# Kernel optimization log

Hardware: AMD Instinct MI355X
Metric: run time of the kernel (lower is better)

## Reference

```python
import jax, jax.numpy as jnp
import numpy as np
from jax import lax

# ---- model dims (from init_kwargs) ----
H_SIZE = 2048      # hidden_size
NK = 16            # linear_num_key_heads
NV = 32            # linear_num_value_heads
DK = 128           # linear_key_head_dim
DV = 128           # linear_value_head_dim
KCONV = 4          # linear_conv_kernel_dim
KEY_DIM = NK * DK          # 2048
VAL_DIM = NV * DV          # 4096
CONV_DIM = 2 * KEY_DIM + VAL_DIM  # 8192
B, S = 2, 2048
EPS = 1e-6


def _l2norm(x, eps=EPS):
    return x * lax.rsqrt(jnp.sum(x * x, axis=-1, keepdims=True) + eps)


def setup_inputs() -> dict:
    key = jax.random.key(0)
    ks = jax.random.split(key, 7)
    x = jax.random.normal(ks[0], (B, S, H_SIZE), jnp.float32)
    W_qkvz = jax.random.normal(ks[1], (2 * KEY_DIM + 2 * VAL_DIM, H_SIZE), jnp.float32) * 0.02
    W_ba = jax.random.normal(ks[2], (2 * NV, H_SIZE), jnp.float32) * 0.02
    conv_w = jax.random.normal(ks[3], (CONV_DIM, 1, KCONV), jnp.float32) * 0.2  # depthwise OIH
    dt_bias = jnp.ones((NV,), jnp.float32)
    A_log = jnp.log(jax.random.uniform(ks[4], (NV,), jnp.float32, 1e-3, 16.0))
    norm_w = jnp.zeros((VAL_DIM,), jnp.float32)
    W_out = jax.random.normal(ks[5], (H_SIZE, VAL_DIM), jnp.float32) * 0.02
    return {"x": x, "W_qkvz": W_qkvz, "W_ba": W_ba, "conv_w": conv_w,
            "dt_bias": dt_bias, "A_log": A_log, "norm_w": norm_w, "W_out": W_out}


def reference(x, W_qkvz, W_ba, conv_w, dt_bias, A_log, norm_w, W_out):
    bs, s, _ = x.shape
    qkvz = jnp.einsum('bsh,ph->bsp', x, W_qkvz)
    ba = jnp.einsum('bsh,ph->bsp', x, W_ba)
    q, k, v, z = jnp.split(qkvz, [KEY_DIM, 2 * KEY_DIM, 2 * KEY_DIM + VAL_DIM], axis=-1)
    b, a = jnp.split(ba, [NV], axis=-1)

    # causal depthwise conv1d over channels (left pad K-1), then SiLU
    mixed = jnp.concatenate([q, k, v], axis=-1).transpose(0, 2, 1)  # [B, CONV_DIM, S]
    mixed = lax.conv_general_dilated(
        mixed, conv_w, window_strides=(1,), padding=[(KCONV - 1, 0)],
        dimension_numbers=('NCH', 'OIH', 'NCH'), feature_group_count=CONV_DIM)
    mixed = jax.nn.silu(mixed).transpose(0, 2, 1)  # [B, S, CONV_DIM]
    q, k, v = jnp.split(mixed, [KEY_DIM, 2 * KEY_DIM], axis=-1)

    q = q.reshape(bs, s, NK, DK)
    k = k.reshape(bs, s, NK, DK)
    v = v.reshape(bs, s, NV, DV)
    beta = jax.nn.sigmoid(b)                                   # [B,S,NV]
    g = -jnp.exp(A_log) * jax.nn.softplus(a + dt_bias)         # [B,S,NV]

    rep = NV // NK
    if rep > 1:
        q = jnp.repeat(q, rep, axis=2)
        k = jnp.repeat(k, rep, axis=2)
    q = _l2norm(q).astype(jnp.float32)
    k = _l2norm(k).astype(jnp.float32)
    v = v.astype(jnp.float32)

    # time-major for scan: [S, B, H, d]
    qs = q.transpose(1, 0, 2, 3)
    ks_ = k.transpose(1, 0, 2, 3)
    vs = v.transpose(1, 0, 2, 3)
    ge = jnp.exp(g).transpose(1, 0, 2)      # [S,B,H]
    bs_ = beta.astype(jnp.float32).transpose(1, 0, 2)  # [S,B,H]

    state0 = jnp.zeros((bs, NV, DK, DV), jnp.float32)

    def step(state, ts):
        q_t, k_t, v_t, g_t, b_t = ts
        state = state * g_t[..., None, None]
        kv_mem = jnp.einsum('bhk,bhkv->bhv', k_t, state)
        delta = b_t[..., None] * (v_t - kv_mem)
        state = state + jnp.einsum('bhk,bhv->bhkv', k_t, delta)
        o_t = jnp.einsum('bhk,bhkv->bhv', q_t, state)
        return state, o_t

    _, core = lax.scan(step, state0, (qs, ks_, vs, ge, bs_))  # core: [S,B,H,DV]
    core = core.transpose(1, 0, 2, 3).reshape(bs, s, VAL_DIM)

    # RMSNorm with (1 + weight) scale
    core = core * lax.rsqrt(jnp.mean(core * core, axis=-1, keepdims=True) + EPS)
    core = core * (1.0 + norm_w)
    core = core * jax.nn.silu(z)
    return jnp.einsum('bsv,hv->bsh', core, W_out)
```

## Files before the change

### kernel.cpp

```cpp
#include <hip/hip_runtime.h>
#include <hip/hip_bf16.h>
#include <math.h>

#define TOK    4096
#define HS     2048
#define CONVD  8192
#define KEYD   2048
#define VALD   4096
#define NKH    16
#define NVH    32
#define DKH    128
#define DVH    128
#define SEQ    2048
#define NBATCH 2
#define EPSF   1e-6f
#define CHUNK  64
#define NCHUNK 32

typedef __attribute__((ext_vector_type(8))) short short8;
typedef __attribute__((ext_vector_type(4))) float floatx4;

static __device__ __forceinline__ unsigned short f2bf(float x) {
  union { float f; unsigned u; } c; c.f = x;
  unsigned r = (c.u + 0x7FFF + ((c.u >> 16) & 1)) >> 16;
  return (unsigned short)r;
}
static __device__ __forceinline__ float bf2f(unsigned short u) {
  union { unsigned u; float f; } c; c.u = ((unsigned)u) << 16;
  return c.f;
}

__global__ __launch_bounds__(256) void gemm_nt(
    const float* __restrict__ A, const float* __restrict__ B,
    float* __restrict__ C, int M, int N, int K) {
  __shared__ float As[16][68];
  __shared__ float Bs[16][68];
  const int tx = threadIdx.x & 15;
  const int ty = threadIdx.x >> 4;
  const int row0 = blockIdx.y * 64;
  const int col0 = blockIdx.x * 64;
  const int lr = threadIdx.x >> 2;
  const int lc = (threadIdx.x & 3) * 4;
  float acc[4][4] = {};
  for (int k0 = 0; k0 < K; k0 += 16) {
    float4 av = *(const float4*)&A[(size_t)(row0 + lr) * K + (k0 + lc)];
    float4 bv = *(const float4*)&B[(size_t)(col0 + lr) * K + (k0 + lc)];
    As[lc + 0][lr] = av.x; As[lc + 1][lr] = av.y;
    As[lc + 2][lr] = av.z; As[lc + 3][lr] = av.w;
    Bs[lc + 0][lr] = bv.x; Bs[lc + 1][lr] = bv.y;
    Bs[lc + 2][lr] = bv.z; Bs[lc + 3][lr] = bv.w;
    __syncthreads();
    #pragma unroll
    for (int kk = 0; kk < 16; kk++) {
      float a[4], b[4];
      #pragma unroll
      for (int i = 0; i < 4; i++) a[i] = As[kk][ty * 4 + i];
      #pragma unroll
      for (int i = 0; i < 4; i++) b[i] = Bs[kk][tx * 4 + i];
      #pragma unroll
      for (int i = 0; i < 4; i++)
        #pragma unroll
        for (int j = 0; j < 4; j++)
          acc[i][j] += a[i] * b[j];
    }
    __syncthreads();
  }
  #pragma unroll
  for (int i = 0; i < 4; i++) {
    float4 v = make_float4(acc[i][0], acc[i][1], acc[i][2], acc[i][3]);
    *(float4*)&C[(size_t)(row0 + ty * 4 + i) * N + (col0 + tx * 4)] = v;
  }
}

__global__ __launch_bounds__(256) void cast_bf16(
    const float4* __restrict__ src, ushort4* __restrict__ dst, int n4) {
  int i = blockIdx.x * 256 + threadIdx.x;
  if (i < n4) {
    float4 v = src[i];
    ushort4 o;
    o.x = f2bf(v.x); o.y = f2bf(v.y); o.z = f2bf(v.z); o.w = f2bf(v.w);
    dst[i] = o;
  }
}

__global__ __launch_bounds__(256) void gemm_bf16_nt(
    const ushort* __restrict__ A, const ushort* __restrict__ B,
    float* __restrict__ C, int M, int N, int K) {
  __shared__ ushort Asm[128 * 32];
  __shared__ ushort Bsm[128 * 32];
  const int tid = threadIdx.x;
  const int w = tid >> 6, l = tid & 63;
  const int row0 = blockIdx.y * 128, col0 = blockIdx.x * 128;
  const int wm = w >> 1, wn = w & 1;

  floatx4 acc[4][4];
  #pragma unroll
  for (int i = 0; i < 4; i++)
    #pragma unroll
    for (int j = 0; j < 4; j++)
      acc[i][j] = (floatx4){0.f, 0.f, 0.f, 0.f};

  const int srow = w * 16 + (l >> 2);
  const int scol = (l & 3) * 8;
  const ushort* Ag = A + (size_t)(row0 + srow) * K + scol;
  const ushort* Bg = B + (size_t)(col0 + srow) * K + scol;

  for (int k0 = 0; k0 < K; k0 += 32) {
    #pragma unroll
    for (int c = 0; c < 2; c++) {
      __builtin_amdgcn_global_load_lds(
          (const __attribute__((address_space(1))) void*)(Ag + (size_t)(c * 64) * K + k0),
          (__attribute__((address_space(3))) void*)&Asm[(c * 64 + w * 16) * 32],
          16, 0, 0);
      __builtin_amdgcn_global_load_lds(
          (const __attribute__((address_space(1))) void*)(Bg + (size_t)(c * 64) * K + k0),
          (__attribute__((address_space(3))) void*)&Bsm[(c * 64 + w * 16) * 32],
          16, 0, 0);
    }
    __syncthreads();
    short8 af[4], bfv[4];
    #pragma unroll
    for (int i = 0; i < 4; i++) {
      af[i]  = *(const short8*)&Asm[(wm * 64 + i * 16 + (l & 15)) * 32 + (l >> 4) * 8];
      bfv[i] = *(const short8*)&Bsm[(wn * 64 + i * 16 + (l & 15)) * 32 + (l >> 4) * 8];
    }
    #pragma unroll
    for (int i = 0; i < 4; i++)
      #pragma unroll
      for (int j = 0; j < 4; j++)
        acc[i][j] = __builtin_amdgcn_mfma_f32_16x16x32_bf16(af[i], bfv[j], acc[i][j], 0, 0, 0);
    __syncthreads();
  }

  const int cl = l & 15, rq = l >> 4;
  #pragma unroll
  for (int i = 0; i < 4; i++) {
    int r0 = row0 + wm * 64 + i * 16 + rq * 4;
    #pragma unroll
    for (int j = 0; j < 4; j++) {
      int cc = col0 + wn * 64 + j * 16 + cl;
      #pragma unroll
      for (int r = 0; r < 4; r++)
        C[(size_t)(r0 + r) * N + cc] = acc[i][j][r];
    }
  }
}

__global__ __launch_bounds__(256) void conv_silu(
    const float* __restrict__ qkv, const float* __restrict__ cw,
    float* __restrict__ mix) {
  size_t idx = (size_t)blockIdx.x * 256 + threadIdx.x;
  int c = (int)(idx % CONVD);
  size_t t = idx / CONVD;
  int s = (int)(t % SEQ);
  float w0 = cw[c * 4 + 0], w1 = cw[c * 4 + 1], w2 = cw[c * 4 + 2], w3 = cw[c * 4 + 3];
  const float* col = qkv + t * CONVD + c;
  float acc = w3 * col[0];
  if (s >= 1) acc += w2 * col[-(ptrdiff_t)CONVD];
  if (s >= 2) acc += w1 * col[-2 * (ptrdiff_t)CONVD];
  if (s >= 3) acc += w0 * col[-3 * (ptrdiff_t)CONVD];
  float sig = 1.f / (1.f + expf(-acc));
  mix[t * CONVD + c] = acc * sig;
}

__global__ __launch_bounds__(256) void gates_kernel(
    const float* __restrict__ ba, const float* __restrict__ A_log,
    const float* __restrict__ dt_bias, float2* __restrict__ g2) {
  int idx = blockIdx.x * 256 + threadIdx.x;
  int h = idx & 31;
  size_t t = (size_t)(idx >> 5);
  float bv = ba[t * 64 + h];
  float av = ba[t * 64 + 32 + h];
  float beta = 1.f / (1.f + expf(-bv));
  float xx = av + dt_bias[h];
  float sp = (xx > 20.f) ? xx : log1pf(expf(xx));
  float lg = -expf(A_log[h]) * sp;
  g2[t * 32 + h] = make_float2(lg, beta);
}

__global__ __launch_bounds__(256) void l2norm_qk(float* __restrict__ mix) {
  int wid = (blockIdx.x * 256 + threadIdx.x) >> 6;
  int lane = threadIdx.x & 63;
  size_t t = (size_t)(wid >> 5);
  int hh = wid & 31;
  float* p = mix + t * CONVD + (size_t)hh * DKH;
  float v0 = p[lane], v1 = p[lane + 64];
  float ss = v0 * v0 + v1 * v1;
  #pragma unroll
  for (int off = 32; off >= 1; off >>= 1) ss += __shfl_xor(ss, off, 64);
  float sc = rsqrtf(ss + EPSF);
  p[lane] = v0 * sc;
  p[lane + 64] = v1 * sc;
}

__global__ __launch_bounds__(64) void chunk_prep(
    const float* __restrict__ mix, const float2* __restrict__ g2,
    float* __restrict__ Lgbuf, ushort* __restrict__ Tbuf,
    ushort* __restrict__ Mbuf) {
  const int blk = blockIdx.x;
  const int ch = blk & 31;
  const int h  = (blk >> 5) & 31;
  const int b  = blk >> 10;
  const int kh = h >> 1;
  const int l  = threadIdx.x;
  const int fr = l & 15;
  const int fc8 = (l >> 4) * 8;
  const int cr = (l >> 4) * 4;

  __shared__ float sLg[64], sB[64];
  __shared__ float sA[64 * 65];
  __shared__ float sT[64 * 65];

  float2 gv = g2[((size_t)(b * SEQ + ch * 64 + l)) * 32 + h];
  float lg = gv.x;
  #pragma unroll
  for (int off = 1; off < 64; off <<= 1) {
    float n = __shfl_up(lg, off, 64);
    if (l >= off) lg += n;
  }
  sLg[l] = lg; sB[l] = gv.y;
  Lgbuf[(size_t)blk * 64 + l] = lg;
  __syncthreads();

  const float* kb = mix + ((size_t)(b * SEQ + ch * 64)) * CONVD + KEYD + (size_t)kh * DKH;
  const float* qb = mix + ((size_t)(b * SEQ + ch * 64)) * CONVD + (size_t)kh * DKH;

  floatx4 zero4 = {0.f, 0.f, 0.f, 0.f};
  floatx4 kk[4][4], qk[4][4];
  #pragma unroll
  for (int i = 0; i < 4; i++)
    #pragma unroll
    for (int j = 0; j < 4; j++) { kk[i][j] = zero4; qk[i][j] = zero4; }

  for (int ks = 0; ks < 4; ks++) {
    short8 kf[4], qf[4];
    #pragma unroll
    for (int m = 0; m < 4; m++) {
      const float* kp = kb + (size_t)(m * 16 + fr) * CONVD + fc8 + ks * 32;
      const float* qp = qb + (size_t)(m * 16 + fr) * CONVD + fc8 + ks * 32;
      float4 a0 = *(const float4*)kp, a1 = *(const float4*)(kp + 4);
      float4 c0 = *(const float4*)qp, c1 = *(const float4*)(qp + 4);
      short8 kv, qv;
      kv[0]=(short)f2bf(a0.x); kv[1]=(short)f2bf(a0.y); kv[2]=(short)f2bf(a0.z); kv[3]=(short)f2bf(a0.w);
      kv[4]=(short)f2bf(a1.x); kv[5]=(short)f2bf(a1.y); kv[6]=(short)f2bf(a1.z); kv[7]=(short)f2bf(a1.w);
      qv[0]=(short)f2bf(c0.x); qv[1]=(short)f2bf(c0.y); qv[2]=(short)f2bf(c0.z); qv[3]=(short)f2bf(c0.w);
      qv[4]=(short)f2bf(c1.x); qv[5]=(short)f2bf(c1.y); qv[6]=(short)f2bf(c1.z); qv[7]=(short)f2bf(c1.w);
      kf[m] = kv; qf[m] = qv;
    }
    #pragma unroll
    for (int mt = 0; mt < 4; mt++)
      #pragma unroll
      for (int nt = 0; nt < 4; nt++) {
        kk[mt][nt] = __builtin_amdgcn_mfma_f32_16x16x32_bf16(kf[mt], kf[nt], kk[mt][nt], 0, 0, 0);
        qk[mt][nt] = __builtin_amdgcn_mfma_f32_16x16x32_bf16(qf[mt], kf[nt], qk[mt][nt], 0, 0, 0);
      }
  }

  const size_t tmbase = (size_t)blk * 4096;
  #pragma unroll
  for (int mt = 0; mt < 4; mt++)
    #pragma unroll
    for (int r = 0; r < 4; r++) {
      int i = mt * 16 + cr + r;
      float Li = sLg[i], Bi = sB[i];
      #pragma unroll
      for (int nt = 0; nt < 4; nt++) {
        int j = nt * 16 + fr;
        float dec = expf(Li - sLg[j]);
        sA[i * 65 + j] = (j < i) ? Bi * dec * kk[mt][nt][r] : 0.f;
        float mv = (j <= i) ? dec * qk[mt][nt][r] : 0.f;
        Mbuf[tmbase + (size_t)i * 64 + j] = f2bf(mv);
      }
    }
  __syncthreads();

  sT[0 * 65 + l] = (l == 0) ? 1.f : 0.f;
  for (int i = 1; i < 64; i++) {
    float acc = (l == i) ? 1.f : 0.f;
    for (int j = 0; j < i; j++)
      acc -= sA[i * 65 + j] * sT[j * 65 + l];
    sT[i * 65 + l] = acc;
  }
  for (int i = 0; i < 64; i++)
    Tbuf[tmbase + (size_t)i * 64 + l] = f2bf(sT[i * 65 + l]);
}

__global__ __launch_bounds__(256) void chunk_scan(
    const float* __restrict__ mix, const float2* __restrict__ g2,
    const float* __restrict__ Lgbuf, const ushort* __restrict__ Tbuf,
    const ushort* __restrict__ Mbuf, float* __restrict__ core) {
  const int blk = blockIdx.x;
  const int vq = blk & 3;
  const int bh = blk >> 2;
  const int h = bh & 31;
  const int b = bh >> 5;
  const int kh = h >> 1;
  const int tid = threadIdx.x;
  const int w = tid >> 6;
  const int l = tid & 63;
  const int fr = l & 15;
  const int fc8 = (l >> 4) * 8;
  const int cr = (l >> 4) * 4;

  __shared__ ushort STh[32][136], STl[32][136];
  __shared__ ushort DTh[32][72],  DTl[32][72];
  __shared__ float sKB[64], sQv[64], sKh[64], sBe[64];
  __shared__ float sLgC;

  for (int i = tid; i < 32 * 136; i += 256) { (&STh[0][0])[i] = 0; (&STl[0][0])[i] = 0; }

  floatx4 zero4 = {0.f, 0.f, 0.f, 0.f};
  floatx4 sacc[2][2] = {{zero4, zero4}, {zero4, zero4}};

  const size_t mixb = (size_t)b * SEQ * CONVD;
  const float* kbase = mix + mixb + KEYD + (size_t)kh * DKH;
  const float* qbase = mix + mixb + (size_t)kh * DKH;
  const float* vbase = mix + mixb + 2 * KEYD + (size_t)h * DVH + vq * 32;
  float* cbase = core + (size_t)b * SEQ * VALD + (size_t)h * DVH + vq * 32;

  for (int ch = 0; ch < NCHUNK; ch++) {
    const int tok0 = ch * 64;
    const size_t tmbase = ((size_t)bh * 32 + ch) * 4096;
    if (tid < 64) {
      float Lgv = Lgbuf[((size_t)bh * 32 + ch) * 64 + tid];
      float LgC = Lgbuf[((size_t)bh * 32 + ch) * 64 + 63];
      float2 gv = g2[((size_t)(b * SEQ + tok0 + tid)) * 32 + h];
      float e = expf(Lgv);
      sKB[tid] = gv.y * e;
      sQv[tid] = e;
      sKh[tid] = expf(LgC - Lgv);
      sBe[tid] = gv.y;
      if (tid == 0) sLgC = LgC;
    }
    __syncthreads();

    const int ia = w * 16 + fr;
    floatx4 p[2] = {zero4, zero4};
    {
      const float* arow = kbase + (size_t)(tok0 + ia) * CONVD;
      float ascl = sKB[ia];
      #pragma unroll
      for (int ks = 0; ks < 4; ks++) {
        float4 x0 = *(const float4*)(arow + fc8 + ks * 32);
        float4 x1 = *(const float4*)(arow + fc8 + ks * 32 + 4);
        short8 af;
        af[0]=(short)f2bf(x0.x*ascl); af[1]=(short)f2bf(x0.y*ascl);
        af[2]=(short)f2bf(x0.z*ascl); af[3]=(short)f2bf(x0.w*ascl);
        af[4]=(short)f2bf(x1.x*ascl); af[5]=(short)f2bf(x1.y*ascl);
        af[6]=(short)f2bf(x1.z*ascl); af[7]=(short)f2bf(x1.w*ascl);
        #pragma unroll
        for (int nt = 0; nt < 2; nt++) {
          short8 bh_ = *(const short8*)&STh[nt * 16 + fr][fc8 + ks * 32];
          short8 bl_ = *(const short8*)&STl[nt * 16 + fr][fc8 + ks * 32];
          p[nt] = __builtin_amdgcn_mfma_f32_16x16x32_bf16(af, bh_, p[nt], 0, 0, 0);
          p[nt] = __builtin_amdgcn_mfma_f32_16x16x32_bf16(af, bl_, p[nt], 0, 0, 0);
        }
      }
    }
    #pragma unroll
    for (int nt = 0; nt < 2; nt++)
      #pragma unroll
      for (int r = 0; r < 4; r++) {
        int i = w * 16 + cr + r;
        int v = nt * 16 + fr;
        float vv = vbase[(size_t)(tok0 + i) * CONVD + v];
        float Rv = sBe[i] * vv - p[nt][r];
        unsigned short hv = f2bf(Rv);
        DTh[v][i] = hv;
        DTl[v][i] = f2bf(Rv - bf2f(hv));
      }
    __syncthreads();

    floatx4 d[2] = {zero4, zero4};
    #pragma unroll
    for (int ks = 0; ks < 2; ks++) {
      short8 af = *(const short8*)&Tbuf[tmbase + (size_t)ia * 64 + fc8 + ks * 32];
      #pragma unroll
      for (int nt = 0; nt < 2; nt++) {
        short8 bh_ = *(const short8*)&DTh[nt * 16 + fr][fc8 + ks * 32];
        short8 bl_ = *(const short8*)&DTl[nt * 16 + fr][fc8 + ks * 32];
        d[nt] = __builtin_amdgcn_mfma_f32_16x16x32_bf16(af, bh_, d[nt], 0, 0, 0);
        d[nt] = __builtin_amdgcn_mfma_f32_16x16x32_bf16(af, bl_, d[nt], 0, 0, 0);
      }
    }
    __syncthreads();
    #pragma unroll
    for (int nt = 0; nt < 2; nt++)
      #pragma unroll
      for (int r = 0; r < 4; r++) {
        int i = w * 16 + cr + r;
        int v = nt * 16 + fr;
        float dv = d[nt][r];
        unsigned short hv = f2bf(dv);
        DTh[v][i] = hv;
        DTl[v][i] = f2bf(dv - bf2f(hv));
      }
    __syncthreads();

    floatx4 o[2] = {zero4, zero4};
    {
      const float* arow = qbase + (size_t)(tok0 + ia) * CONVD;
      float ascl = sQv[ia];
      #pragma unroll
      for (int ks = 0; ks < 4; ks++) {
        float4 x0 = *(const float4*)(arow + fc8 + ks * 32);
        float4 x1 = *(const float4*)(arow + fc8 + ks * 32 + 4);
        short8 af;
        af[0]=(short)f2bf(x0.x*ascl); af[1]=(short)f2bf(x0.y*ascl);
        af[2]=(short)f2bf(x0.z*ascl); af[3]=(short)f2bf(x0.w*ascl);
        af[4]=(short)f2bf(x1.x*ascl); af[5]=(short)f2bf(x1.y*ascl);
        af[6]=(short)f2bf(x1.z*ascl); af[7]=(short)f2bf(x1.w*ascl);
        #pragma unroll
        for (int nt = 0; nt < 2; nt++) {
          short8 bh_ = *(const short8*)&STh[nt * 16 + fr][fc8 + ks * 32];
          short8 bl_ = *(const short8*)&STl[nt * 16 + fr][fc8 + ks * 32];
          o[nt] = __builtin_amdgcn_mfma_f32_16x16x32_bf16(af, bh_, o[nt], 0, 0, 0);
          o[nt] = __builtin_amdgcn_mfma_f32_16x16x32_bf16(af, bl_, o[nt], 0, 0, 0);
        }
      }
      #pragma unroll
      for (int ks = 0; ks < 2; ks++) {
        short8 af = *(const short8*)&Mbuf[tmbase + (size_t)ia * 64 + fc8 + ks * 32];
        #pragma unroll
        for (int nt = 0; nt < 2; nt++) {
          short8 bh_ = *(const short8*)&DTh[nt * 16 + fr][fc8 + ks * 32];
          short8 bl_ = *(const short8*)&DTl[nt * 16 + fr][fc8 + ks * 32];
          o[nt] = __builtin_amdgcn_mfma_f32_16x16x32_bf16(af, bh_, o[nt], 0, 0, 0);
          o[nt] = __builtin_amdgcn_mfma_f32_16x16x32_bf16(af, bl_, o[nt], 0, 0, 0);
        }
      }
    }
    #pragma unroll
    for (int nt = 0; nt < 2; nt++)
      #pragma unroll
      for (int r = 0; r < 4; r++) {
        int i = w * 16 + cr + r;
        int v = nt * 16 + fr;
        cbase[(size_t)(tok0 + i) * VALD + v] = o[nt][r];
      }

    float eL = expf(sLgC);
    #pragma unroll
    for (int mt = 0; mt < 2; mt++)
      #pragma unroll
      for (int nt = 0; nt < 2; nt++)
        sacc[mt][nt] = sacc[mt][nt] * eL;
    #pragma unroll
    for (int ks = 0; ks < 2; ks++) {
      float kh8[8];
      #pragma unroll
      for (int jj = 0; jj < 8; jj++) kh8[jj] = sKh[fc8 + ks * 32 + jj];
      short8 afm[2];
      #pragma unroll
      for (int mt = 0; mt < 2; mt++) {
        int krow = w * 32 + mt * 16 + fr;
        short8 a;
        #pragma unroll
        for (int jj = 0; jj < 8; jj++) {
          float kvv = kbase[(size_t)(tok0 + fc8 + ks * 32 + jj) * CONVD + krow];
          a[jj] = (short)f2bf(kvv * kh8[jj]);
        }
        afm[mt] = a;
      }
      #pragma unroll
      for (int mt = 0; mt < 2; mt++)
        #pragma unroll
        for (int nt = 0; nt < 2; nt++) {
          short8 bh_ = *(const short8*)&DTh[nt * 16 + fr][fc8 + ks * 32];
          short8 bl_ = *(const short8*)&DTl[nt * 16 + fr][fc8 + ks * 32];
          sacc[mt][nt] = __builtin_amdgcn_mfma_f32_16x16x32_bf16(afm[mt], bh_, sacc[mt][nt], 0, 0, 0);
          sacc[mt][nt] = __builtin_amdgcn_mfma_f32_16x16x32_bf16(afm[mt], bl_, sacc[mt][nt], 0, 0, 0);
        }
    }
    __syncthreads();
    #pragma unroll
    for (int mt = 0; mt < 2; mt++)
      #pragma unroll
      for (int nt = 0; nt < 2; nt++)
        #pragma unroll
        for (int r = 0; r < 4; r++) {
          int k = w * 32 + mt * 16 + cr + r;
          int v = nt * 16 + fr;
          float sv = sacc[mt][nt][r];
          unsigned short hv = f2bf(sv);
          STh[v][k] = hv;
          STl[v][k] = f2bf(sv - bf2f(hv));
        }
  }
}

__global__ __launch_bounds__(256) void rmsnorm_silu(
    const float* __restrict__ core, const float* __restrict__ zbuf,
    const float* __restrict__ norm_w, ushort* __restrict__ out_bf) {
  int t = blockIdx.x;
  int tid = threadIdx.x;
  const float* row = core + (size_t)t * VALD;
  const float* zrow = zbuf + (size_t)t * VALD;
  ushort* orow = out_bf + (size_t)t * VALD;
  float vals[16];
  float ss = 0.f;
  #pragma unroll
  for (int i = 0; i < 16; i++) { float x = row[tid + i * 256]; vals[i] = x; ss += x * x; }
  #pragma unroll
  for (int off = 32; off >= 1; off >>= 1) ss += __shfl_xor(ss, off, 64);
  __shared__ float red[4];
  if ((tid & 63) == 0) red[tid >> 6] = ss;
  __syncthreads();
  float tot = red[0] + red[1] + red[2] + red[3];
  float scale = rsqrtf(tot * (1.f / VALD) + EPSF);
  #pragma unroll
  for (int i = 0; i < 16; i++) {
    int c = tid + i * 256;
    float z = zrow[c];
    float sz = z / (1.f + expf(-z));
    orow[c] = f2bf(vals[i] * scale * (1.f + norm_w[c]) * sz);
  }
}

extern "C" void kernel_launch(void* const* d_in, const int* in_sizes, int n_in,
                              void* d_out, int out_size, void* d_ws, size_t ws_size,
                              hipStream_t stream) {
  const float* x       = (const float*)d_in[0];
  const float* W_qkvz  = (const float*)d_in[1];
  const float* W_ba    = (const float*)d_in[2];
  const float* conv_w  = (const float*)d_in[3];
  const float* dt_bias = (const float*)d_in[4];
  const float* A_log   = (const float*)d_in[5];
  const float* norm_w  = (const float*)d_in[6];
  const float* W_out   = (const float*)d_in[7];
  float* out = (float*)d_out;

  float* ws = (float*)d_ws;
  float* A  = ws;
  float* Bp = A + (size_t)33554432;
  float* Cp = Bp + (size_t)33554432;
  float* ba = Cp + (size_t)16777216;
  float* g2 = ba + (size_t)262144;

  ushort* x_bf    = (ushort*)Cp;
  ushort* Wqkv_bf = (ushort*)Bp;
  float*  zb      = A;
  ushort* core_bf = (ushort*)(A + (size_t)16777216);
  ushort* Wz_bf   = (ushort*)(A + (size_t)25165824);
  ushort* Wo_bf   = (ushort*)Bp;
  float*  mix     = Bp;
  float*  core    = Cp;
  ushort* Tbuf    = (ushort*)(A + (size_t)16777216);
  ushort* Mbuf    = (ushort*)(A + (size_t)20971520);
  float*  Lgbuf   = A + (size_t)29360128;

  cast_bf16<<<(TOK * HS / 4 + 255) / 256, 256, 0, stream>>>((const float4*)x, (ushort4*)x_bf, TOK * HS / 4);
  cast_bf16<<<(CONVD * HS / 4 + 255) / 256, 256, 0, stream>>>((const float4*)W_qkvz, (ushort4*)Wqkv_bf, CONVD * HS / 4);
  gemm_bf16_nt<<<dim3(CONVD / 128, TOK / 128), 256, 0, stream>>>(x_bf, Wqkv_bf, A, TOK, CONVD, HS);
  gemm_nt<<<dim3(1, TOK / 64), 256, 0, stream>>>(x, W_ba, ba, TOK, 64, HS);
  conv_silu<<<(int)(((size_t)TOK * CONVD) / 256), 256, 0, stream>>>(A, conv_w, mix);
  cast_bf16<<<(VALD * HS / 4 + 255) / 256, 256, 0, stream>>>(
      (const float4*)(W_qkvz + (size_t)(2 * KEYD + VALD) * HS), (ushort4*)Wz_bf, VALD * HS / 4);
  gemm_bf16_nt<<<dim3(VALD / 128, TOK / 128), 256, 0, stream>>>(x_bf, Wz_bf, zb, TOK, VALD, HS);
  gates_kernel<<<TOK * NVH / 256, 256, 0, stream>>>(ba, A_log, dt_bias, (float2*)g2);
  l2norm_qk<<<TOK * 32 / 4, 256, 0, stream>>>(mix);
  chunk_prep<<<NBATCH * NVH * NCHUNK, 64, 0, stream>>>(mix, (const float2*)g2, Lgbuf, Tbuf, Mbuf);
  chunk_scan<<<NBATCH * NVH * 4, 256, 0, stream>>>(mix, (const float2*)g2, Lgbuf, Tbuf, Mbuf, core);
  rmsnorm_silu<<<TOK, 256, 0, stream>>>(core, zb, norm_w, core_bf);
  cast_bf16<<<(HS * VALD / 4 + 255) / 256, 256, 0, stream>>>((const float4*)W_out, (ushort4*)Wo_bf, HS * VALD / 4);
  gemm_bf16_nt<<<dim3(HS / 128, TOK / 128), 256, 0, stream>>>(core_bf, Wo_bf, out, TOK, HS, VALD);
}
```

Before: 1.188 ms.

## Store normalized q/k as bf16 and software-pipeline chunk_scan with register prefetch

l2norm now writes the normalized q and k to a compact bf16 buffer instead of normalizing in place in fp32. chunk_prep and chunk_scan read that buffer directly, which removes repeated fp32 loads and conversions. chunk_scan is restructured to prefetch the next chunk's K rows and gate values into registers and to load Q/T/M/V early. K is staged in LDS so the transposed state-update reads come from shared memory rather than strided global loads. It also uses lighter barriers, packed LDS stores, and folds the key scaling into the residual, at the cost of extra registers (launch bounds set to one block per SM) and bf16 rounding of q/k before scaling.

Measured after the change: 1.106 ms. 6.9% less time.

```diff
diff --git a/kernel.cpp b/kernel.cpp
--- a/kernel.cpp
+++ b/kernel.cpp
@@ -29,6 +29,13 @@
   union { unsigned u; float f; } c; c.u = ((unsigned)u) << 16;
   return c.f;
 }
+
+#define BAR() do { \
+  __builtin_amdgcn_sched_barrier(0); \
+  asm volatile("s_waitcnt lgkmcnt(0)" ::: "memory"); \
+  __builtin_amdgcn_s_barrier(); \
+  __builtin_amdgcn_sched_barrier(0); \
+} while (0)
 
 __global__ __launch_bounds__(256) void gemm_nt(
     const float* __restrict__ A, const float* __restrict__ B,
@@ -178,23 +185,25 @@
   g2[t * 32 + h] = make_float2(lg, beta);
 }
 
-__global__ __launch_bounds__(256) void l2norm_qk(float* __restrict__ mix) {
+__global__ __launch_bounds__(256) void l2norm_qk(
+    const float* __restrict__ mix, ushort* __restrict__ kq) {
   int wid = (blockIdx.x * 256 + threadIdx.x) >> 6;
   int lane = threadIdx.x & 63;
   size_t t = (size_t)(wid >> 5);
   int hh = wid & 31;
-  float* p = mix + t * CONVD + (size_t)hh * DKH;
+  const float* p = mix + t * CONVD + (size_t)hh * DKH;
   float v0 = p[lane], v1 = p[lane + 64];
   float ss = v0 * v0 + v1 * v1;
   #pragma unroll
   for (int off = 32; off >= 1; off >>= 1) ss += __shfl_xor(ss, off, 64);
   float sc = rsqrtf(ss + EPSF);
-  p[lane] = v0 * sc;
-  p[lane + 64] = v1 * sc;
+  ushort* q = kq + t * 4096 + (size_t)hh * DKH;
+  q[lane] = f2bf(v0 * sc);
+  q[lane + 64] = f2bf(v1 * sc);
 }
 
 __global__ __launch_bounds__(64) void chunk_prep(
-    const float* __restrict__ mix, const float2* __restrict__ g2,
+    const ushort* __restrict__ kq, const float2* __restrict__ g2,
     float* __restrict__ Lgbuf, ushort* __restrict__ Tbuf,
     ushort* __restrict__ Mbuf) {
   const int blk = blockIdx.x;
@@ -222,8 +231,8 @@
   Lgbuf[(size_t)blk * 64 + l] = lg;
   __syncthreads();
 
-  const float* kb = mix + ((size_t)(b * SEQ + ch * 64)) * CONVD + KEYD + (size_t)kh * DKH;
-  const float* qb = mix + ((size_t)(b * SEQ + ch * 64)) * CONVD + (size_t)kh * DKH;
+  const ushort* qb = kq + ((size_t)(b * SEQ + ch * 64)) * 4096 + (size_t)kh * DKH;
+  const ushort* kb = qb + 2048;
 
   floatx4 zero4 = {0.f, 0.f, 0.f, 0.f};
   floatx4 kk[4][4], qk[4][4];
@@ -236,16 +245,8 @@
     short8 kf[4], qf[4];
     #pragma unroll
     for (int m = 0; m < 4; m++) {
-      const float* kp = kb + (size_t)(m * 16 + fr) * CONVD + fc8 + ks * 32;
-      const float* qp = qb + (size_t)(m * 16 + fr) * CONVD + fc8 + ks * 32;
-      float4 a0 = *(const float4*)kp, a1 = *(const float4*)(kp + 4);
-      float4 c0 = *(const float4*)qp, c1 = *(const float4*)(qp + 4);
-      short8 kv, qv;
-      kv[0]=(short)f2bf(a0.x); kv[1]=(short)f2bf(a0.y); kv[2]=(short)f2bf(a0.z); kv[3]=(short)f2bf(a0.w);
-      kv[4]=(short)f2bf(a1.x); kv[5]=(short)f2bf(a1.y); kv[6]=(short)f2bf(a1.z); kv[7]=(short)f2bf(a1.w);
-      qv[0]=(short)f2bf(c0.x); qv[1]=(short)f2bf(c0.y); qv[2]=(short)f2bf(c0.z); qv[3]=(short)f2bf(c0.w);
-      qv[4]=(short)f2bf(c1.x); qv[5]=(short)f2bf(c1.y); qv[6]=(short)f2bf(c1.z); qv[7]=(short)f2bf(c1.w);
-      kf[m] = kv; qf[m] = qv;
+      kf[m] = *(const short8*)(kb + (size_t)(m * 16 + fr) * 4096 + fc8 + ks * 32);
+      qf[m] = *(const short8*)(qb + (size_t)(m * 16 + fr) * 4096 + fc8 + ks * 32);
     }
     #pragma unroll
     for (int mt = 0; mt < 4; mt++)
@@ -285,10 +286,13 @@
     Tbuf[tmbase + (size_t)i * 64 + l] = f2bf(sT[i * 65 + l]);
 }
 
-__global__ __launch_bounds__(256) void chunk_scan(
-    const float* __restrict__ mix, const float2* __restrict__ g2,
-    const float* __restrict__ Lgbuf, const ushort* __restrict__ Tbuf,
-    const ushort* __restrict__ Mbuf, float* __restrict__ core) {
+struct KReg { short8 K[4]; float gLg, gB, gLgC; };
+
+__global__ __launch_bounds__(256, 1) void chunk_scan(
+    const float* __restrict__ mix, const ushort* __restrict__ kq,
+    const float2* __restrict__ g2, const float* __restrict__ Lgbuf,
+    const ushort* __restrict__ Tbuf, const ushort* __restrict__ Mbuf,
+    float* __restrict__ core) {
   const int blk = blockIdx.x;
   const int vq = blk & 3;
   const int bh = blk >> 2;
@@ -301,11 +305,13 @@
   const int fr = l & 15;
   const int fc8 = (l >> 4) * 8;
   const int cr = (l >> 4) * 4;
-
-  __shared__ ushort STh[32][136], STl[32][136];
-  __shared__ ushort DTh[32][72],  DTl[32][72];
-  __shared__ float sKB[64], sQv[64], sKh[64], sBe[64];
-  __shared__ float sLgC;
+  const int w16 = w * 16, w32 = w * 32;
+  const int ia = w16 + fr;
+
+  __shared__ __align__(16) ushort Kt[64][136];
+  __shared__ __align__(16) ushort STh[32][136], STl[32][136];
+  __shared__ __align__(16) ushort DTh[32][72],  DTl[32][72];
+  __shared__ float sKB[64], sQv[64], sKh[64], sBe[64], sLgC[1];
 
   for (int i = tid; i < 32 * 136; i += 256) { (&STh[0][0])[i] = 0; (&STl[0][0])[i] = 0; }
 
@@ -313,152 +319,160 @@
   floatx4 sacc[2][2] = {{zero4, zero4}, {zero4, zero4}};
 
   const size_t mixb = (size_t)b * SEQ * CONVD;
-  const float* kbase = mix + mixb + KEYD + (size_t)kh * DKH;
-  const float* qbase = mix + mixb + (size_t)kh * DKH;
-  const float* vbase = mix + mixb + 2 * KEYD + (size_t)h * DVH + vq * 32;
+  const float* vb = mix + mixb + 2 * KEYD + (size_t)h * DVH + vq * 32;
+  const ushort* kq_q = kq + (size_t)b * SEQ * 4096 + (size_t)kh * DKH;
+  const ushort* kq_k = kq_q + 2048;
+  const ushort* Tb = Tbuf + (size_t)bh * 32 * 4096;
+  const ushort* Mb = Mbuf + (size_t)bh * 32 * 4096;
+  const float* Lgb = Lgbuf + (size_t)bh * 2048;
+  const float2* gp = g2 + (size_t)b * SEQ * 32 + h;
   float* cbase = core + (size_t)b * SEQ * VALD + (size_t)h * DVH + vq * 32;
 
-  for (int ch = 0; ch < NCHUNK; ch++) {
+  auto kpre = [&](KReg& R, int ch) {
+    size_t ro = (size_t)(ch * 64 + ia) * 4096;
+    #pragma unroll
+    for (int ks = 0; ks < 4; ks++)
+      R.K[ks] = *(const short8*)(kq_k + ro + fc8 + ks * 32);
+    if (tid < 64) {
+      R.gLg = Lgb[ch * 64 + tid];
+      R.gLgC = Lgb[ch * 64 + 63];
+      R.gB = gp[(size_t)(ch * 64 + tid) * 32].y;
+    }
+  };
+
+  auto body = [&](KReg& cur, KReg& nxt, int ch) {
     const int tok0 = ch * 64;
-    const size_t tmbase = ((size_t)bh * 32 + ch) * 4096;
     if (tid < 64) {
-      float Lgv = Lgbuf[((size_t)bh * 32 + ch) * 64 + tid];
-      float LgC = Lgbuf[((size_t)bh * 32 + ch) * 64 + 63];
-      float2 gv = g2[((size_t)(b * SEQ + tok0 + tid)) * 32 + h];
-      float e = expf(Lgv);
-      sKB[tid] = gv.y * e;
+      float e = expf(cur.gLg);
+      sKB[tid] = cur.gB * e;
       sQv[tid] = e;
-      sKh[tid] = expf(LgC - Lgv);
-      sBe[tid] = gv.y;
-      if (tid == 0) sLgC = LgC;
-    }
-    __syncthreads();
-
-    const int ia = w * 16 + fr;
+      sKh[tid] = expf(cur.gLgC - cur.gLg);
+      sBe[tid] = cur.gB;
+      if (tid == 0) sLgC[0] = cur.gLgC;
+    }
+    #pragma unroll
+    for (int ks = 0; ks < 4; ks++)
+      *(short8*)&Kt[ia][fc8 + ks * 32] = cur.K[ks];
+    short8 Qr[4], Tr[2], Mr[2];
+    float Vr[8];
+    {
+      size_t ro = (size_t)(tok0 + ia) * 4096;
+      #pragma unroll
+      for (int ks = 0; ks < 4; ks++)
+        Qr[ks] = *(const short8*)(kq_q + ro + fc8 + ks * 32);
+      size_t tmb = (size_t)ch * 4096 + (size_t)ia * 64;
+      #pragma unroll
+      for (int ks = 0; ks < 2; ks++) {
+        Tr[ks] = *(const short8*)(Tb + tmb + fc8 + ks * 32);
+        Mr[ks] = *(const short8*)(Mb + tmb + fc8 + ks * 32);
+      }
+      #pragma unroll
+      for (int nt = 0; nt < 2; nt++)
+        #pragma unroll
+        for (int r = 0; r < 4; r++)
+          Vr[nt * 4 + r] = vb[(size_t)(tok0 + w16 + cr + r) * CONVD + nt * 16 + fr];
+    }
+    BAR();
+    kpre(nxt, (ch + 1 < NCHUNK) ? ch + 1 : NCHUNK - 1);
+
     floatx4 p[2] = {zero4, zero4};
-    {
-      const float* arow = kbase + (size_t)(tok0 + ia) * CONVD;
-      float ascl = sKB[ia];
-      #pragma unroll
-      for (int ks = 0; ks < 4; ks++) {
-        float4 x0 = *(const float4*)(arow + fc8 + ks * 32);
-        float4 x1 = *(const float4*)(arow + fc8 + ks * 32 + 4);
-        short8 af;
-        af[0]=(short)f2bf(x0.x*ascl); af[1]=(short)f2bf(x0.y*ascl);
-        af[2]=(short)f2bf(x0.z*ascl); af[3]=(short)f2bf(x0.w*ascl);
-        af[4]=(short)f2bf(x1.x*ascl); af[5]=(short)f2bf(x1.y*ascl);
-        af[6]=(short)f2bf(x1.z*ascl); af[7]=(short)f2bf(x1.w*ascl);
-        #pragma unroll
-        for (int nt = 0; nt < 2; nt++) {
-          short8 bh_ = *(const short8*)&STh[nt * 16 + fr][fc8 + ks * 32];
-          short8 bl_ = *(const short8*)&STl[nt * 16 + fr][fc8 + ks * 32];
-          p[nt] = __builtin_amdgcn_mfma_f32_16x16x32_bf16(af, bh_, p[nt], 0, 0, 0);
-          p[nt] = __builtin_amdgcn_mfma_f32_16x16x32_bf16(af, bl_, p[nt], 0, 0, 0);
-        }
-      }
-    }
-    #pragma unroll
-    for (int nt = 0; nt < 2; nt++)
+    #pragma unroll
+    for (int ks = 0; ks < 4; ks++)
+      #pragma unroll
+      for (int nt = 0; nt < 2; nt++) {
+        short8 bh_ = *(const short8*)&STh[nt * 16 + fr][fc8 + ks * 32];
+        short8 bl_ = *(const short8*)&STl[nt * 16 + fr][fc8 + ks * 32];
+        p[nt] = __builtin_amdgcn_mfma_f32_16x16x32_bf16(cur.K[ks], bh_, p[nt], 0, 0, 0);
+        p[nt] = __builtin_amdgcn_mfma_f32_16x16x32_bf16(cur.K[ks], bl_, p[nt], 0, 0, 0);
+      }
+    #pragma unroll
+    for (int nt = 0; nt < 2; nt++) {
+      unsigned hv[4], lv[4];
       #pragma unroll
       for (int r = 0; r < 4; r++) {
-        int i = w * 16 + cr + r;
-        int v = nt * 16 + fr;
-        float vv = vbase[(size_t)(tok0 + i) * CONVD + v];
-        float Rv = sBe[i] * vv - p[nt][r];
-        unsigned short hv = f2bf(Rv);
-        DTh[v][i] = hv;
-        DTl[v][i] = f2bf(Rv - bf2f(hv));
-      }
-    __syncthreads();
+        int i = w16 + cr + r;
+        float Rv = sBe[i] * Vr[nt * 4 + r] - sKB[i] * p[nt][r];
+        unsigned short hq = f2bf(Rv);
+        hv[r] = hq; lv[r] = f2bf(Rv - bf2f(hq));
+      }
+      int v = nt * 16 + fr;
+      *(uint2*)&DTh[v][w16 + cr] = make_uint2(hv[0] | (hv[1] << 16), hv[2] | (hv[3] << 16));
+      *(uint2*)&DTl[v][w16 + cr] = make_uint2(lv[0] | (lv[1] << 16), lv[2] | (lv[3] << 16));
+    }
+    BAR();
 
     floatx4 d[2] = {zero4, zero4};
     #pragma unroll
-    for (int ks = 0; ks < 2; ks++) {
-      short8 af = *(const short8*)&Tbuf[tmbase + (size_t)ia * 64 + fc8 + ks * 32];
+    for (int ks = 0; ks < 2; ks++)
       #pragma unroll
       for (int nt = 0; nt < 2; nt++) {
         short8 bh_ = *(const short8*)&DTh[nt * 16 + fr][fc8 + ks * 32];
         short8 bl_ = *(const short8*)&DTl[nt * 16 + fr][fc8 + ks * 32];
-        d[nt] = __builtin_amdgcn_mfma_f32_16x16x32_bf16(af, bh_, d[nt], 0, 0, 0);
-        d[nt] = __builtin_amdgcn_mfma_f32_16x16x32_bf16(af, bl_, d[nt], 0, 0, 0);
-      }
-    }
-    __syncthreads();
+        d[nt] = __builtin_amdgcn_mfma_f32_16x16x32_bf16(Tr[ks], bh_, d[nt], 0, 0, 0);
+        d[nt] = __builtin_amdgcn_mfma_f32_16x16x32_bf16(Tr[ks], bl_, d[nt], 0, 0, 0);
+      }
+    BAR();
+    #pragma unroll
+    for (int nt = 0; nt < 2; nt++) {
+      unsigned hv[4], lv[4];
+      #pragma unroll
+      for (int r = 0; r < 4; r++) {
+        float dv = d[nt][r];
+        unsigned short hq = f2bf(dv);
+        hv[r] = hq; lv[r] = f2bf(dv - bf2f(hq));
+      }
+      int v = nt * 16 + fr;
+      *(uint2*)&DTh[v][w16 + cr] = make_uint2(hv[0] | (hv[1] << 16), hv[2] | (hv[3] << 16));
+      *(uint2*)&DTl[v][w16 + cr] = make_uint2(lv[0] | (lv[1] << 16), lv[2] | (lv[3] << 16));
+    }
+    BAR();
+
+    floatx4 oq[2] = {zero4, zero4}, od[2] = {zero4, zero4};
+    #pragma unroll
+    for (int ks = 0; ks < 4; ks++)
+      #pragma unroll
+      for (int nt = 0; nt < 2; nt++) {
+        short8 bh_ = *(const short8*)&STh[nt * 16 + fr][fc8 + ks * 32];
+        short8 bl_ = *(const short8*)&STl[nt * 16 + fr][fc8 + ks * 32];
+        oq[nt] = __builtin_amdgcn_mfma_f32_16x16x32_bf16(Qr[ks], bh_, oq[nt], 0, 0, 0);
+        oq[nt] = __builtin_amdgcn_mfma_f32_16x16x32_bf16(Qr[ks], bl_, oq[nt], 0, 0, 0);
+      }
+    #pragma unroll
+    for (int ks = 0; ks < 2; ks++)
+      #pragma unroll
+      for (int nt = 0; nt < 2; nt++) {
+        short8 bh_ = *(const short8*)&DTh[nt * 16 + fr][fc8 + ks * 32];
+        short8 bl_ = *(const short8*)&DTl[nt * 16 + fr][fc8 + ks * 32];
+        od[nt] = __builtin_amdgcn_mfma_f32_16x16x32_bf16(Mr[ks], bh_, od[nt], 0, 0, 0);
+        od[nt] = __builtin_amdgcn_mfma_f32_16x16x32_bf16(Mr[ks], bl_, od[nt], 0, 0, 0);
+      }
     #pragma unroll
     for (int nt = 0; nt < 2; nt++)
       #pragma unroll
       for (int r = 0; r < 4; r++) {
-        int i = w * 16 + cr + r;
-        int v = nt * 16 + fr;
-        float dv = d[nt][r];
-        unsigned short hv = f2bf(dv);
-        DTh[v][i] = hv;
-        DTl[v][i] = f2bf(dv - bf2f(hv));
-      }
-    __syncthreads();
-
-    floatx4 o[2] = {zero4, zero4};
-    {
-      const float* arow = qbase + (size_t)(tok0 + ia) * CONVD;
-      float ascl = sQv[ia];
-      #pragma unroll
-      for (int ks = 0; ks < 4; ks++) {
-        float4 x0 = *(const float4*)(arow + fc8 + ks * 32);
-        float4 x1 = *(const float4*)(arow + fc8 + ks * 32 + 4);
-        short8 af;
-        af[0]=(short)f2bf(x0.x*ascl); af[1]=(short)f2bf(x0.y*ascl);
-        af[2]=(short)f2bf(x0.z*ascl); af[3]=(short)f2bf(x0.w*ascl);
-        af[4]=(short)f2bf(x1.x*ascl); af[5]=(short)f2bf(x1.y*ascl);
-        af[6]=(short)f2bf(x1.z*ascl); af[7]=(short)f2bf(x1.w*ascl);
+        int i = w16 + cr + r;
+        cbase[(size_t)(tok0 + i) * VALD + nt * 16 + fr] = sQv[i] * oq[nt][r] + od[nt][r];
+      }
+
+    float eL = expf(sLgC[0]);
+    #pragma unroll
+    for (int mt = 0; mt < 2; mt++)
+      #pragma unroll
+      for (int nt = 0; nt < 2; nt++)
         #pragma unroll
-        for (int nt = 0; nt < 2; nt++) {
-          short8 bh_ = *(const short8*)&STh[nt * 16 + fr][fc8 + ks * 32];
-          short8 bl_ = *(const short8*)&STl[nt * 16 + fr][fc8 + ks * 32];
-          o[nt] = __builtin_amdgcn_mfma_f32_16x16x32_bf16(af, bh_, o[nt], 0, 0, 0);
-          o[nt] = __builtin_amdgcn_mfma_f32_16x16x32_bf16(af, bl_, o[nt], 0, 0, 0);
-        }
-      }
-      #pragma unroll
-      for (int ks = 0; ks < 2; ks++) {
-        short8 af = *(const short8*)&Mbuf[tmbase + (size_t)ia * 64 + fc8 + ks * 32];
-        #pragma unroll
-        for (int nt = 0; nt < 2; nt++) {
-          short8 bh_ = *(const short8*)&DTh[nt * 16 + fr][fc8 + ks * 32];
-          short8 bl_ = *(const short8*)&DTl[nt * 16 + fr][fc8 + ks * 32];
-          o[nt] = __builtin_amdgcn_mfma_f32_16x16x32_bf16(af, bh_, o[nt], 0, 0, 0);
-          o[nt] = __builtin_amdgcn_mfma_f32_16x16x32_bf16(af, bl_, o[nt], 0, 0, 0);
-        }
-      }
-    }
-    #pragma unroll
-    for (int nt = 0; nt < 2; nt++)
-      #pragma unroll
-      for (int r = 0; r < 4; r++) {
-        int i = w * 16 + cr + r;
-        int v = nt * 16 + fr;
-        cbase[(size_t)(tok0 + i) * VALD + v] = o[nt][r];
-      }
-
-    float eL = expf(sLgC);
-    #pragma unroll
-    for (int mt = 0; mt < 2; mt++)
-      #pragma unroll
-      for (int nt = 0; nt < 2; nt++)
-        sacc[mt][nt] = sacc[mt][nt] * eL;
+        for (int r = 0; r < 4; r++)
+          sacc[mt][nt][r] *= eL;
     #pragma unroll
     for (int ks = 0; ks < 2; ks++) {
-      float kh8[8];
-      #pragma unroll
-      for (int jj = 0; jj < 8; jj++) kh8[jj] = sKh[fc8 + ks * 32 + jj];
       short8 afm[2];
       #pragma unroll
       for (int mt = 0; mt < 2; mt++) {
-        int krow = w * 32 + mt * 16 + fr;
         short8 a;
         #pragma unroll
         for (int jj = 0; jj < 8; jj++) {
-          float kvv = kbase[(size_t)(tok0 + fc8 + ks * 32 + jj) * CONVD + krow];
-          a[jj] = (short)f2bf(kvv * kh8[jj]);
+          int tk = fc8 + ks * 32 + jj;
+          float kv = bf2f(Kt[tk][w32 + mt * 16 + fr]);
+          a[jj] = (short)f2bf(kv * sKh[tk]);
         }
         afm[mt] = a;
       }
@@ -472,20 +486,32 @@
           sacc[mt][nt] = __builtin_amdgcn_mfma_f32_16x16x32_bf16(afm[mt], bl_, sacc[mt][nt], 0, 0, 0);
         }
     }
-    __syncthreads();
+    BAR();
     #pragma unroll
     for (int mt = 0; mt < 2; mt++)
       #pragma unroll
-      for (int nt = 0; nt < 2; nt++)
+      for (int nt = 0; nt < 2; nt++) {
+        unsigned hv[4], lv[4];
         #pragma unroll
         for (int r = 0; r < 4; r++) {
-          int k = w * 32 + mt * 16 + cr + r;
-          int v = nt * 16 + fr;
           float sv = sacc[mt][nt][r];
-          unsigned short hv = f2bf(sv);
-          STh[v][k] = hv;
-          STl[v][k] = f2bf(sv - bf2f(hv));
+          unsigned short hq = f2bf(sv);
+          hv[r] = hq; lv[r] = f2bf(sv - bf2f(hq));
         }
+        int v = nt * 16 + fr, k0 = w32 + mt * 16 + cr;
+        *(uint2*)&STh[v][k0] = make_uint2(hv[0] | (hv[1] << 16), hv[2] | (hv[3] << 16));
+        *(uint2*)&STl[v][k0] = make_uint2(lv[0] | (lv[1] << 16), lv[2] | (lv[3] << 16));
+      }
+  };
+
+  KReg RA, RB;
+  RA.gLg = RA.gB = RA.gLgC = 0.f;
+  RB.gLg = RB.gB = RB.gLgC = 0.f;
+  kpre(RA, 0);
+  #pragma unroll 1
+  for (int ch = 0; ch < NCHUNK; ch += 2) {
+    body(RA, RB, ch);
+    body(RB, RA, ch + 1);
   }
 }
 
@@ -547,7 +573,8 @@
   float*  core    = Cp;
   ushort* Tbuf    = (ushort*)(A + (size_t)16777216);
   ushort* Mbuf    = (ushort*)(A + (size_t)20971520);
-  float*  Lgbuf   = A + (size_t)29360128;
+  ushort* kq_bf   = (ushort*)(A + (size_t)25165824);
+  float*  Lgbuf   = ba;
 
   cast_bf16<<<(TOK * HS / 4 + 255) / 256, 256, 0, stream>>>((const float4*)x, (ushort4*)x_bf, TOK * HS / 4);
   cast_bf16<<<(CONVD * HS / 4 + 255) / 256, 256, 0, stream>>>((const float4*)W_qkvz, (ushort4*)Wqkv_bf, CONVD * HS / 4);
@@ -558,9 +585,9 @@
       (const float4*)(W_qkvz + (size_t)(2 * KEYD + VALD) * HS), (ushort4*)Wz_bf, VALD * HS / 4);
   gemm_bf16_nt<<<dim3(VALD / 128, TOK / 128), 256, 0, stream>>>(x_bf, Wz_bf, zb, TOK, VALD, HS);
   gates_kernel<<<TOK * NVH / 256, 256, 0, stream>>>(ba, A_log, dt_bias, (float2*)g2);
-  l2norm_qk<<<TOK * 32 / 4, 256, 0, stream>>>(mix);
-  chunk_prep<<<NBATCH * NVH * NCHUNK, 64, 0, stream>>>(mix, (const float2*)g2, Lgbuf, Tbuf, Mbuf);
-  chunk_scan<<<NBATCH * NVH * 4, 256, 0, stream>>>(mix, (const float2*)g2, Lgbuf, Tbuf, Mbuf, core);
+  l2norm_qk<<<TOK * 32 / 4, 256, 0, stream>>>(mix, kq_bf);
+  chunk_prep<<<NBATCH * NVH * NCHUNK, 64, 0, stream>>>(kq_bf, (const float2*)g2, Lgbuf, Tbuf, Mbuf);
+  chunk_scan<<<NBATCH * NVH * 4, 256, 0, stream>>>(mix, kq_bf, (const float2*)g2, Lgbuf, Tbuf, Mbuf, core);
   rmsnorm_silu<<<TOK, 256, 0, stream>>>(core, zb, norm_w, core_bf);
   cast_bf16<<<(HS * VALD / 4 + 255) / 256, 256, 0, stream>>>((const float4*)W_out, (ushort4*)Wo_bf, HS * VALD / 4);
   gemm_bf16_nt<<<dim3(HS / 128, TOK / 128), 256, 0, stream>>>(core_bf, Wo_bf, out, TOK, HS, VALD);
```
